# Kernel tuning notes

Measured on AMD Instinct MI355X. Metric: run time of the kernel, lower is better.

Reference implementation:

```python
import jax, jax.numpy as jnp
import numpy as np

NEG_INF = -9e15
ALPHA = 0.2  # LeakyReLU negative slope


def setup_inputs() -> dict:
    key = jax.random.key(0)
    k1, k2, k3, k4 = jax.random.split(key, 4)
    N, F_in, F_out = 8192, 128, 64
    h = jax.random.normal(k1, (N, F_in), dtype=jnp.float32)
    adj = jax.random.randint(k2, (N, N), 0, 2, dtype=jnp.int32)
    W = jax.random.normal(k3, (F_in, F_out), dtype=jnp.float32) * (1.414 / np.sqrt(F_in))
    a = jax.random.normal(k4, (2 * F_out, 1), dtype=jnp.float32) * 0.1
    return {"h": h, "adj": adj, "W": W, "a": a}


def reference(h, adj, W, a):
    # Wh: [N, F_out]
    Wh = h @ W
    F_out = Wh.shape[1]
    # Decomposed additive score: cat([Wh_i, Wh_j]) @ a == Wh_i@a1 + Wh_j@a2.
    # Identical math to the original repeat/cat/mm, without the [N*N, 2F] blowup.
    s1 = Wh @ a[:F_out, 0]   # [N] source-side score
    s2 = Wh @ a[F_out:, 0]   # [N] target-side score
    e = jax.nn.leaky_relu(s1[:, None] + s2[None, :], negative_slope=ALPHA)  # [N, N]
    attention = jax.nn.softmax(jnp.where(adj > 0, e, NEG_INF), axis=1)
    # dropout is identity in eval mode
    h_prime = attention @ Wh  # [N, F_out]
    return (h_prime, attention)
```

## Files before the change

kernel.cpp:

```cpp
#include <hip/hip_runtime.h>

#define NN 8192
#define FIN 128
#define FOUT 64
#define NEGINF (-9e15f)
#define LALPHA 0.2f

typedef float f32x4 __attribute__((ext_vector_type(4)));
typedef short short8 __attribute__((ext_vector_type(8)));
typedef unsigned long long ull;

__device__ __forceinline__ unsigned short f32_to_bf16(float x) {
  unsigned int u = __float_as_uint(x);
  u = (u + 0x7fffu + ((u >> 16) & 1u)) >> 16;
  return (unsigned short)u;
}
__device__ __forceinline__ float bf16_to_f32(unsigned short b) {
  return __uint_as_float(((unsigned int)b) << 16);
}

__global__ __launch_bounds__(256) void gat_prep(
    const float* __restrict__ h, const float* __restrict__ W,
    const float* __restrict__ a,
    float* __restrict__ s1g, float* __restrict__ s2g,
    unsigned short* __restrict__ whfh)
{
  __shared__ __align__(16) float Wl[FIN * FOUT];
  __shared__ __align__(16) float hl[16 * FIN];
  const int tid = threadIdx.x;
  const int i0 = blockIdx.x * 16;
  #pragma unroll
  for (int it = 0; it < 8; ++it) {
    int idx = (it * 256 + tid) * 4;
    *(f32x4*)&Wl[idx] = *(const f32x4*)&W[idx];
  }
  #pragma unroll
  for (int it = 0; it < 2; ++it) {
    int idx = (it * 256 + tid) * 4;
    *(f32x4*)&hl[idx] = *(const f32x4*)&h[(size_t)i0 * FIN + idx];
  }
  __syncthreads();
  const int r = tid >> 4;
  const int f0 = (tid & 15) * 4;
  f32x4 acc = {0.f, 0.f, 0.f, 0.f};
  #pragma unroll 8
  for (int k = 0; k < FIN; ++k) {
    float hv = hl[r * FIN + k];
    f32x4 wv = *(const f32x4*)&Wl[k * FOUT + f0];
    acc += hv * wv;
  }
  f32x4 a1v = *(const f32x4*)&a[f0];
  f32x4 a2v = *(const f32x4*)&a[FOUT + f0];
  float p1 = acc.x * a1v.x + acc.y * a1v.y + acc.z * a1v.z + acc.w * a1v.w;
  float p2 = acc.x * a2v.x + acc.y * a2v.y + acc.z * a2v.z + acc.w * a2v.w;
  #pragma unroll
  for (int d = 1; d < 16; d <<= 1) {
    p1 += __shfl_xor(p1, d, 16);
    p2 += __shfl_xor(p2, d, 16);
  }
  const int j = i0 + r;
  if ((tid & 15) == 0) { s1g[j] = p1; s2g[j] = p2; }
  const int kstep = j >> 5;
  const int lhi = (j >> 3) & 3;
  const int ein = j & 7;
  #pragma unroll
  for (int e = 0; e < 4; ++e) {
    int f = f0 + e;
    unsigned short hb = f32_to_bf16(acc[e]);
    int ln = lhi * 16 + (f & 15);
    whfh[(size_t)(kstep * 4 + (f >> 4)) * 512 + ln * 8 + ein] = hb;
  }
}

__global__ __launch_bounds__(1024, 8) void gat_fused(
    const int* __restrict__ adj,
    const float* __restrict__ s1g, const float* __restrict__ s2g,
    const unsigned short* __restrict__ whfh,
    float* __restrict__ outh, float* __restrict__ outa)
{
  __shared__ __align__(16) float s2l[NN];
  __shared__ __align__(16) unsigned int maskl[16][258];
  __shared__ float rowp[16][3];
  const int tid = threadIdx.x;
  const int lane = tid & 63;
  const int wv = tid >> 6;
  const int i0 = blockIdx.x * 16;

  #pragma unroll
  for (int it = 0; it < 2; ++it) {
    int idx = (it * 1024 + tid) * 4;
    *(f32x4*)&s2l[idx] = *(const f32x4*)&s2g[idx];
  }
  __syncthreads();

  {
    const float s1v = s1g[i0 + wv];
    const float M = fmaxf(s1v, LALPHA * s1v);
    const int* __restrict__ ar = adj + (size_t)(i0 + wv) * NN;
    float ls = 0.f;
    #pragma unroll 4
    for (int it = 0; it < 128; ++it) {
      int jj = it * 64 + lane;
      int a0 = __builtin_nontemporal_load(&ar[jj]);
      float sv = s2l[jj];
      ull b = __ballot(a0 > 0);
      float x = s1v + sv;
      x = fmaxf(x, LALPHA * x);
      float e = __expf(x - M);
      ls += (a0 > 0) ? e : 0.f;
      if (lane == 0) *(ull*)&maskl[wv][it * 2] = b;
    }
    #pragma unroll
    for (int d = 1; d < 64; d <<= 1) ls += __shfl_xor(ls, d);
    if (lane == 0) {
      rowp[wv][0] = s1v; rowp[wv][1] = M; rowp[wv][2] = 1.f / ls;
    }
  }
  __syncthreads();

  const int row = lane & 15;
  const int kg = lane >> 4;
  const float s1r = rowp[row][0];
  const float mr = rowp[row][1];
  const float rir = rowp[row][2];
  const int kbase = wv * 512;
  f32x4 acc0 = {0,0,0,0}, acc1 = {0,0,0,0}, acc2 = {0,0,0,0}, acc3 = {0,0,0,0};
  float* __restrict__ orow = outa + (size_t)(i0 + row) * NN;
  const short8* __restrict__ bfrag = (const short8*)whfh;
  for (int step = 0; step < 16; ++step) {
    const int k0 = kbase + step * 32;
    const int jb = k0 + kg * 8;
    f32x4 sa = *(const f32x4*)&s2l[jb];
    f32x4 sb = *(const f32x4*)&s2l[jb + 4];
    unsigned int bits = maskl[row][k0 >> 5] >> (kg * 8);
    float s2v[8] = {sa.x, sa.y, sa.z, sa.w, sb.x, sb.y, sb.z, sb.w};
    float af[8];
    short8 AH, AL;
    #pragma unroll
    for (int e = 0; e < 8; ++e) {
      float x = s1r + s2v[e];
      x = fmaxf(x, LALPHA * x);
      x = ((bits >> e) & 1u) ? x : NEGINF;
      float p = __expf(x - mr) * rir;
      af[e] = p;
      unsigned short hb = f32_to_bf16(p);
      AH[e] = (short)hb;
      AL[e] = (short)f32_to_bf16(p - bf16_to_f32(hb));
    }
    f32x4 st0 = {af[0], af[1], af[2], af[3]};
    f32x4 st1 = {af[4], af[5], af[6], af[7]};
    *(f32x4*)&orow[jb] = st0;
    *(f32x4*)&orow[jb + 4] = st1;
    size_t fb = (size_t)(k0 >> 5) * 256 + lane;
    short8 B0 = bfrag[fb];
    short8 B1 = bfrag[fb + 64];
    short8 B2 = bfrag[fb + 128];
    short8 B3 = bfrag[fb + 192];
    acc0 = __builtin_amdgcn_mfma_f32_16x16x32_bf16(AH, B0, acc0, 0, 0, 0);
    acc1 = __builtin_amdgcn_mfma_f32_16x16x32_bf16(AH, B1, acc1, 0, 0, 0);
    acc2 = __builtin_amdgcn_mfma_f32_16x16x32_bf16(AH, B2, acc2, 0, 0, 0);
    acc3 = __builtin_amdgcn_mfma_f32_16x16x32_bf16(AH, B3, acc3, 0, 0, 0);
    acc0 = __builtin_amdgcn_mfma_f32_16x16x32_bf16(AL, B0, acc0, 0, 0, 0);
    acc1 = __builtin_amdgcn_mfma_f32_16x16x32_bf16(AL, B1, acc1, 0, 0, 0);
    acc2 = __builtin_amdgcn_mfma_f32_16x16x32_bf16(AL, B2, acc2, 0, 0, 0);
    acc3 = __builtin_amdgcn_mfma_f32_16x16x32_bf16(AL, B3, acc3, 0, 0, 0);
  }
  __syncthreads();
  float* red = (float*)&maskl[0][0];
  const int c15 = lane & 15;
  f32x4 av[4] = {acc0, acc1, acc2, acc3};
  float* slab = red + (wv & 3) * 1024;
  if (wv < 4) {
    #pragma unroll
    for (int nt = 0; nt < 4; ++nt)
      #pragma unroll
      for (int rg = 0; rg < 4; ++rg)
        slab[(kg * 4 + rg) * 64 + nt * 16 + c15] = av[nt][rg];
  }
  __syncthreads();
  if (wv >= 4 && wv < 8) {
    #pragma unroll
    for (int nt = 0; nt < 4; ++nt)
      #pragma unroll
      for (int rg = 0; rg < 4; ++rg)
        slab[(kg * 4 + rg) * 64 + nt * 16 + c15] += av[nt][rg];
  }
  __syncthreads();
  if (wv >= 8 && wv < 12) {
    #pragma unroll
    for (int nt = 0; nt < 4; ++nt)
      #pragma unroll
      for (int rg = 0; rg < 4; ++rg)
        slab[(kg * 4 + rg) * 64 + nt * 16 + c15] += av[nt][rg];
  }
  __syncthreads();
  if (wv >= 12) {
    #pragma unroll
    for (int nt = 0; nt < 4; ++nt)
      #pragma unroll
      for (int rg = 0; rg < 4; ++rg)
        slab[(kg * 4 + rg) * 64 + nt * 16 + c15] += av[nt][rg];
  }
  __syncthreads();
  outh[(size_t)i0 * FOUT + tid] =
      red[tid] + red[1024 + tid] + red[2048 + tid] + red[3072 + tid];
}

extern "C" void kernel_launch(void* const* d_in, const int* in_sizes, int n_in,
                              void* d_out, int out_size, void* d_ws, size_t ws_size,
                              hipStream_t stream) {
  const float* h = (const float*)d_in[0];
  const int* adj = (const int*)d_in[1];
  const float* W = (const float*)d_in[2];
  const float* a = (const float*)d_in[3];
  float* outh = (float*)d_out;
  float* outa = outh + (size_t)NN * FOUT;
  char* ws = (char*)d_ws;
  float* s1g = (float*)ws;
  float* s2g = s1g + NN;
  unsigned short* whfh = (unsigned short*)(ws + 128 * 1024);
  gat_prep<<<512, 256, 0, stream>>>(h, W, a, s1g, s2g, whfh);
  gat_fused<<<512, 1024, 0, stream>>>(adj, s1g, s2g, whfh, outh, outa);
}
```

Baseline: 507.0 us.

## Process two row groups per block, overlapping adj scan with softmax-matmul

Each block now handles 32 rows instead of 16, split into two groups. The first half of the waves runs the softmax and MFMA phase for group 0 while the second half scans the adjacency rows for group 1. The roles then swap, so adjacency streaming overlaps with exponent, store and MFMA work inside one block. This halves the grid, doubles the per-wave k range, adds shared memory for the second mask and reduction buffers, and lowers the launch-bounds occupancy hint, which may cost latency hiding.

```diff
diff --git a/kernel.cpp b/kernel.cpp
--- a/kernel.cpp
+++ b/kernel.cpp
@@ -7,6 +7,7 @@
 #define LALPHA 0.2f
 
 typedef float f32x4 __attribute__((ext_vector_type(4)));
+typedef float f32x2 __attribute__((ext_vector_type(2)));
 typedef short short8 __attribute__((ext_vector_type(8)));
 typedef unsigned long long ull;
 
@@ -72,19 +73,20 @@
   }
 }
 
-__global__ __launch_bounds__(1024, 8) void gat_fused(
+__global__ __launch_bounds__(1024, 4) void gat_fused(
     const int* __restrict__ adj,
     const float* __restrict__ s1g, const float* __restrict__ s2g,
     const unsigned short* __restrict__ whfh,
     float* __restrict__ outh, float* __restrict__ outa)
 {
   __shared__ __align__(16) float s2l[NN];
-  __shared__ __align__(16) unsigned int maskl[16][258];
-  __shared__ float rowp[16][3];
+  __shared__ __align__(16) unsigned int maskl[2][16][258];
+  __shared__ __align__(16) float red[4][1024];
+  __shared__ float rowp[2][16][3];
   const int tid = threadIdx.x;
   const int lane = tid & 63;
   const int wv = tid >> 6;
-  const int i0 = blockIdx.x * 16;
+  const int i0 = blockIdx.x * 32;
 
   #pragma unroll
   for (int it = 0; it < 2; ++it) {
@@ -108,102 +110,179 @@
       x = fmaxf(x, LALPHA * x);
       float e = __expf(x - M);
       ls += (a0 > 0) ? e : 0.f;
-      if (lane == 0) *(ull*)&maskl[wv][it * 2] = b;
+      if (lane == 0) *(ull*)&maskl[0][wv][it * 2] = b;
     }
     #pragma unroll
     for (int d = 1; d < 64; d <<= 1) ls += __shfl_xor(ls, d);
     if (lane == 0) {
-      rowp[wv][0] = s1v; rowp[wv][1] = M; rowp[wv][2] = 1.f / ls;
-    }
-  }
-  __syncthreads();
-
-  const int row = lane & 15;
+      rowp[0][wv][0] = s1v; rowp[0][wv][1] = M; rowp[0][wv][2] = 1.f / ls;
+    }
+  }
+  __syncthreads();
+
+  const int arow = lane & 15;
   const int kg = lane >> 4;
-  const float s1r = rowp[row][0];
-  const float mr = rowp[row][1];
-  const float rir = rowp[row][2];
-  const int kbase = wv * 512;
   f32x4 acc0 = {0,0,0,0}, acc1 = {0,0,0,0}, acc2 = {0,0,0,0}, acc3 = {0,0,0,0};
-  float* __restrict__ orow = outa + (size_t)(i0 + row) * NN;
   const short8* __restrict__ bfrag = (const short8*)whfh;
-  for (int step = 0; step < 16; ++step) {
-    const int k0 = kbase + step * 32;
-    const int jb = k0 + kg * 8;
-    f32x4 sa = *(const f32x4*)&s2l[jb];
-    f32x4 sb = *(const f32x4*)&s2l[jb + 4];
-    unsigned int bits = maskl[row][k0 >> 5] >> (kg * 8);
-    float s2v[8] = {sa.x, sa.y, sa.z, sa.w, sb.x, sb.y, sb.z, sb.w};
-    float af[8];
-    short8 AH, AL;
+
+  auto runP2 = [&](int g, int kbase) {
+    const float s1r = rowp[g][arow][0];
+    const float mr  = rowp[g][arow][1];
+    const float rir = rowp[g][arow][2];
+    float* __restrict__ orow = outa + (size_t)(i0 + g * 16 + arow) * NN;
+    for (int step = 0; step < 16; ++step) {
+      const int k0 = kbase + step * 64;
+      #pragma unroll
+      for (int half = 0; half < 2; ++half) {
+        const int kh = k0 + half * 32;
+        const int jb = kh + kg * 8;
+        f32x4 sa = *(const f32x4*)&s2l[jb];
+        f32x4 sb = *(const f32x4*)&s2l[jb + 4];
+        unsigned int bits = maskl[g][arow][kh >> 5] >> (kg * 8);
+        float s2v[8] = {sa.x, sa.y, sa.z, sa.w, sb.x, sb.y, sb.z, sb.w};
+        float af[8];
+        short8 AH, AL;
+        #pragma unroll
+        for (int e = 0; e < 8; ++e) {
+          float x = s1r + s2v[e];
+          x = fmaxf(x, LALPHA * x);
+          x = ((bits >> e) & 1u) ? x : NEGINF;
+          float p = __expf(x - mr) * rir;
+          af[e] = p;
+          unsigned short hb = f32_to_bf16(p);
+          AH[e] = (short)hb;
+          AL[e] = (short)f32_to_bf16(p - bf16_to_f32(hb));
+        }
+        f32x4 st0 = {af[0], af[1], af[2], af[3]};
+        f32x4 st1 = {af[4], af[5], af[6], af[7]};
+        *(f32x4*)&orow[jb] = st0;
+        *(f32x4*)&orow[jb + 4] = st1;
+        size_t fb = (size_t)(kh >> 5) * 256 + lane;
+        short8 B0 = bfrag[fb];
+        short8 B1 = bfrag[fb + 64];
+        short8 B2 = bfrag[fb + 128];
+        short8 B3 = bfrag[fb + 192];
+        acc0 = __builtin_amdgcn_mfma_f32_16x16x32_bf16(AH, B0, acc0, 0, 0, 0);
+        acc1 = __builtin_amdgcn_mfma_f32_16x16x32_bf16(AH, B1, acc1, 0, 0, 0);
+        acc2 = __builtin_amdgcn_mfma_f32_16x16x32_bf16(AH, B2, acc2, 0, 0, 0);
+        acc3 = __builtin_amdgcn_mfma_f32_16x16x32_bf16(AH, B3, acc3, 0, 0, 0);
+        acc0 = __builtin_amdgcn_mfma_f32_16x16x32_bf16(AL, B0, acc0, 0, 0, 0);
+        acc1 = __builtin_amdgcn_mfma_f32_16x16x32_bf16(AL, B1, acc1, 0, 0, 0);
+        acc2 = __builtin_amdgcn_mfma_f32_16x16x32_bf16(AL, B2, acc2, 0, 0, 0);
+        acc3 = __builtin_amdgcn_mfma_f32_16x16x32_bf16(AL, B3, acc3, 0, 0, 0);
+      }
+    }
+  };
+
+  if (wv < 8) {
+    runP2(0, wv * 1024);
+  } else {
+    const int rl0 = (wv - 8) * 2, rl1 = rl0 + 1;
+    const float s1a = s1g[i0 + 16 + rl0];
+    const float s1b = s1g[i0 + 16 + rl1];
+    const float Ma = fmaxf(s1a, LALPHA * s1a);
+    const float Mb = fmaxf(s1b, LALPHA * s1b);
+    const int* __restrict__ ara = adj + (size_t)(i0 + 16 + rl0) * NN;
+    const int* __restrict__ arb = adj + (size_t)(i0 + 16 + rl1) * NN;
+    float la = 0.f, lb = 0.f;
+    #pragma unroll 2
+    for (int it = 0; it < 128; ++it) {
+      int jj = it * 64 + lane;
+      int a0 = __builtin_nontemporal_load(&ara[jj]);
+      int a1 = __builtin_nontemporal_load(&arb[jj]);
+      float sv = s2l[jj];
+      ull b0 = __ballot(a0 > 0);
+      ull b1 = __ballot(a1 > 0);
+      float xa = s1a + sv; xa = fmaxf(xa, LALPHA * xa);
+      float xb = s1b + sv; xb = fmaxf(xb, LALPHA * xb);
+      la += (a0 > 0) ? __expf(xa - Ma) : 0.f;
+      lb += (a1 > 0) ? __expf(xb - Mb) : 0.f;
+      if (lane == 0) {
+        *(ull*)&maskl[1][rl0][it * 2] = b0;
+        *(ull*)&maskl[1][rl1][it * 2] = b1;
+      }
+    }
     #pragma unroll
-    for (int e = 0; e < 8; ++e) {
-      float x = s1r + s2v[e];
-      x = fmaxf(x, LALPHA * x);
-      x = ((bits >> e) & 1u) ? x : NEGINF;
-      float p = __expf(x - mr) * rir;
-      af[e] = p;
-      unsigned short hb = f32_to_bf16(p);
-      AH[e] = (short)hb;
-      AL[e] = (short)f32_to_bf16(p - bf16_to_f32(hb));
-    }
-    f32x4 st0 = {af[0], af[1], af[2], af[3]};
-    f32x4 st1 = {af[4], af[5], af[6], af[7]};
-    *(f32x4*)&orow[jb] = st0;
-    *(f32x4*)&orow[jb + 4] = st1;
-    size_t fb = (size_t)(k0 >> 5) * 256 + lane;
-    short8 B0 = bfrag[fb];
-    short8 B1 = bfrag[fb + 64];
-    short8 B2 = bfrag[fb + 128];
-    short8 B3 = bfrag[fb + 192];
-    acc0 = __builtin_amdgcn_mfma_f32_16x16x32_bf16(AH, B0, acc0, 0, 0, 0);
-    acc1 = __builtin_amdgcn_mfma_f32_16x16x32_bf16(AH, B1, acc1, 0, 0, 0);
-    acc2 = __builtin_amdgcn_mfma_f32_16x16x32_bf16(AH, B2, acc2, 0, 0, 0);
-    acc3 = __builtin_amdgcn_mfma_f32_16x16x32_bf16(AH, B3, acc3, 0, 0, 0);
-    acc0 = __builtin_amdgcn_mfma_f32_16x16x32_bf16(AL, B0, acc0, 0, 0, 0);
-    acc1 = __builtin_amdgcn_mfma_f32_16x16x32_bf16(AL, B1, acc1, 0, 0, 0);
-    acc2 = __builtin_amdgcn_mfma_f32_16x16x32_bf16(AL, B2, acc2, 0, 0, 0);
-    acc3 = __builtin_amdgcn_mfma_f32_16x16x32_bf16(AL, B3, acc3, 0, 0, 0);
-  }
-  __syncthreads();
-  float* red = (float*)&maskl[0][0];
-  const int c15 = lane & 15;
-  f32x4 av[4] = {acc0, acc1, acc2, acc3};
-  float* slab = red + (wv & 3) * 1024;
-  if (wv < 4) {
-    #pragma unroll
-    for (int nt = 0; nt < 4; ++nt)
-      #pragma unroll
-      for (int rg = 0; rg < 4; ++rg)
-        slab[(kg * 4 + rg) * 64 + nt * 16 + c15] = av[nt][rg];
-  }
-  __syncthreads();
-  if (wv >= 4 && wv < 8) {
-    #pragma unroll
-    for (int nt = 0; nt < 4; ++nt)
-      #pragma unroll
-      for (int rg = 0; rg < 4; ++rg)
-        slab[(kg * 4 + rg) * 64 + nt * 16 + c15] += av[nt][rg];
-  }
-  __syncthreads();
-  if (wv >= 8 && wv < 12) {
-    #pragma unroll
-    for (int nt = 0; nt < 4; ++nt)
-      #pragma unroll
-      for (int rg = 0; rg < 4; ++rg)
-        slab[(kg * 4 + rg) * 64 + nt * 16 + c15] += av[nt][rg];
-  }
-  __syncthreads();
-  if (wv >= 12) {
-    #pragma unroll
-    for (int nt = 0; nt < 4; ++nt)
-      #pragma unroll
-      for (int rg = 0; rg < 4; ++rg)
-        slab[(kg * 4 + rg) * 64 + nt * 16 + c15] += av[nt][rg];
-  }
-  __syncthreads();
-  outh[(size_t)i0 * FOUT + tid] =
-      red[tid] + red[1024 + tid] + red[2048 + tid] + red[3072 + tid];
+    for (int d = 1; d < 64; d <<= 1) {
+      la += __shfl_xor(la, d);
+      lb += __shfl_xor(lb, d);
+    }
+    if (lane == 0) {
+      rowp[1][rl0][0] = s1a; rowp[1][rl0][1] = Ma; rowp[1][rl0][2] = 1.f / la;
+      rowp[1][rl1][0] = s1b; rowp[1][rl1][1] = Mb; rowp[1][rl1][2] = 1.f / lb;
+    }
+  }
+  __syncthreads();
+
+  {
+    f32x4 av[4] = {acc0, acc1, acc2, acc3};
+    float* slab = &red[wv & 3][0];
+    if (wv < 4) {
+      #pragma unroll
+      for (int nt = 0; nt < 4; ++nt)
+        #pragma unroll
+        for (int rg = 0; rg < 4; ++rg)
+          slab[(kg * 4 + rg) * 64 + nt * 16 + arow] = av[nt][rg];
+    }
+  }
+  __syncthreads();
+  {
+    f32x4 av[4] = {acc0, acc1, acc2, acc3};
+    float* slab = &red[wv & 3][0];
+    if (wv >= 4 && wv < 8) {
+      #pragma unroll
+      for (int nt = 0; nt < 4; ++nt)
+        #pragma unroll
+        for (int rg = 0; rg < 4; ++rg)
+          slab[(kg * 4 + rg) * 64 + nt * 16 + arow] += av[nt][rg];
+    }
+  }
+  __syncthreads();
+  if (tid < 512) {
+    int base = tid * 2;
+    f32x2 r0 = *(f32x2*)&red[0][base];
+    f32x2 r1 = *(f32x2*)&red[1][base];
+    f32x2 r2 = *(f32x2*)&red[2][base];
+    f32x2 r3 = *(f32x2*)&red[3][base];
+    f32x2 s = r0 + r1 + r2 + r3;
+    *(f32x2*)&outh[(size_t)i0 * FOUT + base] = s;
+  }
+
+  if (wv >= 8) runP2(1, (wv - 8) * 1024);
+  __syncthreads();
+  {
+    f32x4 av[4] = {acc0, acc1, acc2, acc3};
+    float* slab = &red[wv & 3][0];
+    if (wv >= 8 && wv < 12) {
+      #pragma unroll
+      for (int nt = 0; nt < 4; ++nt)
+        #pragma unroll
+        for (int rg = 0; rg < 4; ++rg)
+          slab[(kg * 4 + rg) * 64 + nt * 16 + arow] = av[nt][rg];
+    }
+  }
+  __syncthreads();
+  {
+    f32x4 av[4] = {acc0, acc1, acc2, acc3};
+    float* slab = &red[wv & 3][0];
+    if (wv >= 12) {
+      #pragma unroll
+      for (int nt = 0; nt < 4; ++nt)
+        #pragma unroll
+        for (int rg = 0; rg < 4; ++rg)
+          slab[(kg * 4 + rg) * 64 + nt * 16 + arow] += av[nt][rg];
+    }
+  }
+  __syncthreads();
+  if (tid >= 512) {
+    int base = (tid - 512) * 2;
+    f32x2 r0 = *(f32x2*)&red[0][base];
+    f32x2 r1 = *(f32x2*)&red[1][base];
+    f32x2 r2 = *(f32x2*)&red[2][base];
+    f32x2 r3 = *(f32x2*)&red[3][base];
+    f32x2 s = r0 + r1 + r2 + r3;
+    *(f32x2*)&outh[(size_t)(i0 + 16) * FOUT + base] = s;
+  }
 }
 
 extern "C" void kernel_launch(void* const* d_in, const int* in_sizes, int n_in,
@@ -220,5 +299,5 @@
   float* s2g = s1g + NN;
   unsigned short* whfh = (unsigned short*)(ws + 128 * 1024);
   gat_prep<<<512, 256, 0, stream>>>(h, W, a, s1g, s2g, whfh);
-  gat_fused<<<512, 1024, 0, stream>>>(adj, s1g, s2g, whfh, outh, outa);
-}
+  gat_fused<<<256, 1024, 0, stream>>>(adj, s1g, s2g, whfh, outh, outa);
+}
```

Result: slower. 581.3 us (+14.6%).
